# Kernel optimization log

Measured on AMD Instinct MI355X. Metric: run time of the kernel, lower is better.

The kernel has to match this reference:

```python
import jax, jax.numpy as jnp
import numpy as np

DIM = 1024
NUM_HEADS = 16
HEAD_DIM = DIM // NUM_HEADS
MLP_HIDDEN = 4 * DIM
SCALE = HEAD_DIM ** -0.5
EPS = 1e-5


def setup_inputs() -> dict:
    key = jax.random.key(0)
    ks = jax.random.split(key, 6)
    s = (2.0 / DIM) ** 0.5
    sd = (2.0 / MLP_HIDDEN) ** 0.5
    return {
        "x": jax.random.normal(ks[0], (2, 2048, DIM), dtype=jnp.float32),
        "attn_qkv_weight": jax.random.normal(ks[1], (3 * DIM, DIM), dtype=jnp.float32) * s,
        "attn_out_weight": jax.random.normal(ks[2], (DIM, DIM), dtype=jnp.float32) * s,
        "norm1_weight": jnp.ones((DIM,), jnp.float32),
        "norm1_bias": jnp.zeros((DIM,), jnp.float32),
        "mlp_gate_weight": jax.random.normal(ks[3], (MLP_HIDDEN, DIM), dtype=jnp.float32) * s,
        "mlp_up_weight": jax.random.normal(ks[4], (MLP_HIDDEN, DIM), dtype=jnp.float32) * s,
        "mlp_down_weight": jax.random.normal(ks[5], (DIM, MLP_HIDDEN), dtype=jnp.float32) * sd,
        "norm2_weight": jnp.ones((DIM,), jnp.float32),
        "norm2_bias": jnp.zeros((DIM,), jnp.float32),
    }


def _layer_norm(x, w, b):
    mean = x.mean(axis=-1, keepdims=True)
    var = jnp.mean(jnp.square(x - mean), axis=-1, keepdims=True)
    return (x - mean) / jnp.sqrt(var + EPS) * w + b


def reference(x, attn_qkv_weight, attn_out_weight, norm1_weight, norm1_bias,
              mlp_gate_weight, mlp_up_weight, mlp_down_weight, norm2_weight, norm2_bias):
    B, S, D = x.shape
    residual1 = x
    xn = _layer_norm(x, norm1_weight, norm1_bias)
    qkv = xn @ attn_qkv_weight.T                      # [B,S,3D]
    qkv = qkv.reshape(B, S, 3, NUM_HEADS, HEAD_DIM).transpose(2, 0, 3, 1, 4)
    q, k, v = qkv[0], qkv[1], qkv[2]                  # [B,H,S,hd]
    scores = jnp.einsum('bhqd,bhkd->bhqk', q, k) * SCALE  # full O(S^2) matrix
    attn = jax.nn.softmax(scores, axis=-1)            # no causal mask (default False)
    out = jnp.einsum('bhqk,bhkd->bhqd', attn, v)      # [B,H,S,hd]
    out = out.transpose(0, 2, 1, 3).reshape(B, S, D)
    x2 = residual1 + out @ attn_out_weight.T
    xn2 = _layer_norm(x2, norm2_weight, norm2_bias)
    gate = xn2 @ mlp_gate_weight.T
    up = xn2 @ mlp_up_weight.T
    hidden = jax.nn.silu(gate) * up
    return x2 + hidden @ mlp_down_weight.T
```

## Files before the change

### kernel.cpp

```cpp
#include <hip/hip_runtime.h>

typedef float f32x4 __attribute__((ext_vector_type(4)));
typedef __bf16 bf16x8 __attribute__((ext_vector_type(8)));
typedef unsigned int u32;

#define DEV __device__ __forceinline__
#define WAITVM(n) asm volatile("s_waitcnt vmcnt(" #n ")" ::: "memory")

DEV void gload_lds16(const void* g, void* l) {
  __builtin_amdgcn_global_load_lds(
      (const __attribute__((address_space(1))) u32*)g,
      (__attribute__((address_space(3))) u32*)l, 16, 0, 0);
}

DEV int xcd_swz(int flat, int nwg) {
  return (flat & 7) * (nwg >> 3) + (flat >> 3);
}

__global__ __launch_bounds__(256) void cvt_bf16(const float* __restrict__ in,
                                                __bf16* __restrict__ o, int n) {
  int i = (blockIdx.x * 256 + threadIdx.x) * 8;
  if (i >= n) return;
  float4 a = *(const float4*)(in + i);
  float4 b = *(const float4*)(in + i + 4);
  union { bf16x8 v; __bf16 e[8]; } u;
  u.e[0] = (__bf16)a.x; u.e[1] = (__bf16)a.y; u.e[2] = (__bf16)a.z; u.e[3] = (__bf16)a.w;
  u.e[4] = (__bf16)b.x; u.e[5] = (__bf16)b.y; u.e[6] = (__bf16)b.z; u.e[7] = (__bf16)b.w;
  *(bf16x8*)(o + i) = u.v;
}

__global__ __launch_bounds__(256) void ln_kernel(const float* __restrict__ x,
                                                 const float* __restrict__ w,
                                                 const float* __restrict__ b,
                                                 __bf16* __restrict__ o) {
  const int row = blockIdx.x, tid = threadIdx.x;
  const float4 v = ((const float4*)(x + (size_t)row * 1024))[tid];
  float s  = v.x + v.y + v.z + v.w;
  float s2 = v.x * v.x + v.y * v.y + v.z * v.z + v.w * v.w;
  for (int off = 32; off; off >>= 1) {
    s  += __shfl_down(s, off);
    s2 += __shfl_down(s2, off);
  }
  __shared__ float rs[4], rs2[4];
  if ((tid & 63) == 0) { rs[tid >> 6] = s; rs2[tid >> 6] = s2; }
  __syncthreads();
  float S = rs[0] + rs[1] + rs[2] + rs[3];
  float S2 = rs2[0] + rs2[1] + rs2[2] + rs2[3];
  float mean = S * (1.0f / 1024.0f);
  float var = S2 * (1.0f / 1024.0f) - mean * mean;
  float inv = rsqrtf(var + 1e-5f);
  const float4 wv = ((const float4*)w)[tid];
  const float4 bv = ((const float4*)b)[tid];
  union { ushort4 u4; __bf16 e[4]; } u;
  u.e[0] = (__bf16)((v.x - mean) * inv * wv.x + bv.x);
  u.e[1] = (__bf16)((v.y - mean) * inv * wv.y + bv.y);
  u.e[2] = (__bf16)((v.z - mean) * inv * wv.z + bv.z);
  u.e[3] = (__bf16)((v.w - mean) * inv * wv.w + bv.w);
  *(ushort4*)(o + (size_t)row * 1024 + tid * 4) = u.u4;
}


template <int EPI, int MI>
__global__ __launch_bounds__(256) void gemm_bt(const __bf16* __restrict__ A,
                                               const __bf16* __restrict__ B,
                                               void* __restrict__ Cout,
                                               const float* __restrict__ Res,
                                               int M, int N, int K) {
  constexpr int BM = MI * 32;
  constexpr int L = MI / 2 + 2;
  __shared__ __align__(16) __bf16 As[2][BM * 32];
  __shared__ __align__(16) __bf16 Bs[2][128 * 32];
  const int tid = threadIdx.x;
  const int lane = tid & 63;
  const int w = tid >> 6;
  const int wr = w >> 1, wc = w & 1;
  const int l15 = lane & 15, g = lane >> 4;

  const int nbx = gridDim.x;
  const int logical = xcd_swz(blockIdx.y * nbx + blockIdx.x, nbx * gridDim.y);
  const int per = 8 * nbx, grp = logical / per, rem = logical % per;
  const int bm = (grp * 8 + (rem & 7)) * BM;
  const int bn = (rem >> 3) * 128;

  f32x4 acc[MI][4] = {};

  auto stage = [&](int buf, int k0) {
#pragma unroll
    for (int p = 0; p < MI / 2; ++p) {
      const int ch = p * 256 + tid;
      const int S = ch >> 6, u = ch & 63;
      gload_lds16(A + (size_t)(bm + S * 16 + (u & 15)) * K + k0 + (u >> 4) * 8,
                  &As[buf][(p * 256 + w * 64) * 8]);
    }
#pragma unroll
    for (int p = 0; p < 2; ++p) {
      const int ch = p * 256 + tid;
      const int S = ch >> 6, u = ch & 63;
      gload_lds16(B + (size_t)(bn + S * 16 + (u & 15)) * K + k0 + (u >> 4) * 8,
                  &Bs[buf][(p * 256 + w * 64) * 8]);
    }
  };

  const int NT = K >> 5;
  stage(0, 0);
  stage(1, 32);

  for (int t = 0; t < NT; ++t) {
    if (t + 1 < NT) {
      if (L == 3) WAITVM(3); else WAITVM(4);
    } else {
      WAITVM(0);
    }
    __syncthreads();
    const int cur = t & 1;
    bf16x8 af[MI], bfr[4];
#pragma unroll
    for (int i = 0; i < MI; ++i)
      af[i] = *(const bf16x8*)(&As[cur][(wr * MI + i) * 512 + lane * 8]);
#pragma unroll
    for (int j = 0; j < 4; ++j)
      bfr[j] = *(const bf16x8*)(&Bs[cur][(wc * 4 + j) * 512 + lane * 8]);
#pragma unroll
    for (int i = 0; i < MI; ++i)
#pragma unroll
      for (int j = 0; j < 4; ++j)
        acc[i][j] = __builtin_amdgcn_mfma_f32_16x16x32_bf16(af[i], bfr[j], acc[i][j], 0, 0, 0);
    __syncthreads();
    if (t + 2 < NT) stage(cur, (t + 2) * 32);
  }

  const int r0 = bm + wr * (MI * 16) + g * 4;
  const int c0 = bn + wc * 64 + l15;
#pragma unroll
  for (int i = 0; i < MI; ++i)
#pragma unroll
    for (int j = 0; j < 4; ++j)
#pragma unroll
      for (int r = 0; r < 4; ++r) {
        const size_t idx = (size_t)(r0 + i * 16 + r) * N + (c0 + j * 16);
        const float v = acc[i][j][r];
        if (EPI == 0) ((__bf16*)Cout)[idx] = (__bf16)v;
        else          ((float*)Cout)[idx] = v + Res[idx];
      }
}

__global__ __launch_bounds__(256, 2) void gemm_mlp(const __bf16* __restrict__ A,
                                                   const __bf16* __restrict__ BG,
                                                   const __bf16* __restrict__ BU,
                                                   __bf16* __restrict__ H,
                                                   int M, int N, int K) {
  __shared__ __align__(16) __bf16 As[2][128 * 32];
  __shared__ __align__(16) __bf16 Bg[2][128 * 32];
  __shared__ __align__(16) __bf16 Bu[2][128 * 32];
  const int tid = threadIdx.x;
  const int lane = tid & 63;
  const int w = tid >> 6;
  const int wr = w >> 1, wc = w & 1;
  const int l15 = lane & 15, g = lane >> 4;

  const int nbx = gridDim.x;
  const int logical = xcd_swz(blockIdx.y * nbx + blockIdx.x, nbx * gridDim.y);
  const int per = 8 * nbx, grp = logical / per, rem = logical % per;
  const int bm = (grp * 8 + (rem & 7)) * 128;
  const int bn = (rem >> 3) * 128;

  f32x4 accg[4][4] = {};
  f32x4 accu[4][4] = {};

  auto stage = [&](int buf, int k0) {
#pragma unroll
    for (int p = 0; p < 2; ++p) {
      const int ch = p * 256 + tid;
      const int S = ch >> 6, u = ch & 63;
      const size_t roff = (size_t)(S * 16 + (u & 15));
      const int coff = (u >> 4) * 8;
      const int dst = (p * 256 + w * 64) * 8;
      gload_lds16(A + ((size_t)bm + roff) * K + k0 + coff, &As[buf][dst]);
      gload_lds16(BG + ((size_t)bn + roff) * K + k0 + coff, &Bg[buf][dst]);
      gload_lds16(BU + ((size_t)bn + roff) * K + k0 + coff, &Bu[buf][dst]);
    }
  };

  const int NT = K >> 5;
  stage(0, 0);
  stage(1, 32);

  for (int t = 0; t < NT; ++t) {
    if (t + 1 < NT) { WAITVM(6); } else { WAITVM(0); }
    __syncthreads();
    const int cur = t & 1;
    bf16x8 af[4], bgf[4], buf_[4];
#pragma unroll
    for (int i = 0; i < 4; ++i)
      af[i] = *(const bf16x8*)(&As[cur][(wr * 4 + i) * 512 + lane * 8]);
#pragma unroll
    for (int j = 0; j < 4; ++j) {
      bgf[j] = *(const bf16x8*)(&Bg[cur][(wc * 4 + j) * 512 + lane * 8]);
      buf_[j] = *(const bf16x8*)(&Bu[cur][(wc * 4 + j) * 512 + lane * 8]);
    }
#pragma unroll
    for (int i = 0; i < 4; ++i)
#pragma unroll
      for (int j = 0; j < 4; ++j) {
        accg[i][j] = __builtin_amdgcn_mfma_f32_16x16x32_bf16(af[i], bgf[j], accg[i][j], 0, 0, 0);
        accu[i][j] = __builtin_amdgcn_mfma_f32_16x16x32_bf16(af[i], buf_[j], accu[i][j], 0, 0, 0);
      }
    __syncthreads();
    if (t + 2 < NT) stage(cur, (t + 2) * 32);
  }

  const int r0 = bm + wr * 64 + g * 4;
  const int c0 = bn + wc * 64 + l15;
#pragma unroll
  for (int i = 0; i < 4; ++i)
#pragma unroll
    for (int j = 0; j < 4; ++j)
#pragma unroll
      for (int r = 0; r < 4; ++r) {
        const float gt = accg[i][j][r];
        const float ut = accu[i][j][r];
        const float h = gt / (1.0f + __expf(-gt)) * ut;
        H[(size_t)(r0 + i * 16 + r) * N + (c0 + j * 16)] = (__bf16)h;
      }
}

__global__ __launch_bounds__(256) void transpose_v(const __bf16* __restrict__ qkv,
                                                   __bf16* __restrict__ vT) {
  const int st = blockIdx.x, bh = blockIdx.y;
  const int b = bh >> 4, h = bh & 15;
  __shared__ __bf16 tile[64][80];
  const int tid = threadIdx.x;
#pragma unroll
  for (int it = 0; it < 2; ++it) {
    const int idx = it * 256 + tid;
    const int r = idx >> 3, c0 = (idx & 7) * 8;
    bf16x8 v = *(const bf16x8*)(qkv + (size_t)(b * 2048 + st * 64 + r) * 3072 + 2048 + h * 64 + c0);
    *(bf16x8*)&tile[r][c0] = v;
  }
  __syncthreads();
#pragma unroll
  for (int it = 0; it < 2; ++it) {
    const int idx = it * 256 + tid;
    const int d = idx >> 3, s0 = (idx & 7) * 8;
    union { bf16x8 v; __bf16 e[8]; } u;
#pragma unroll
    for (int j = 0; j < 8; ++j) u.e[j] = tile[s0 + j][d];
    *(bf16x8*)(vT + (size_t)(bh * 64 + d) * 2048 + st * 64 + s0) = u.v;
  }
}

__global__ __launch_bounds__(256) void attn_kernel(const __bf16* __restrict__ qkv,
                                                   const __bf16* __restrict__ vT,
                                                   __bf16* __restrict__ outp) {
  const int logical = xcd_swz(blockIdx.y * 32 + blockIdx.x, 1024);
  const int qt = logical & 31, bh = logical >> 5;
  const int b = bh >> 4, h = bh & 15;
  const int tid = threadIdx.x, lane = tid & 63, w = tid >> 6;
  const int l15 = lane & 15, g = lane >> 4;
  const float CSC = 0.125f * 1.44269504f;

  __shared__ __align__(16) __bf16 Ks[64 * 64];
  __shared__ __align__(16) __bf16 Vs[64 * 64];
  __shared__ __align__(16) __bf16 Ps[4][16 * 80];

  const int qrow = qt * 64 + w * 16 + l15;
  const size_t qbase = (size_t)(b * 2048 + qrow) * 3072 + h * 64;
  const bf16x8 qf0 = *(const bf16x8*)(qkv + qbase + g * 8);
  const bf16x8 qf1 = *(const bf16x8*)(qkv + qbase + 32 + g * 8);

  f32x4 o_acc[4] = {};
  float l_r[4] = {0.f, 0.f, 0.f, 0.f};

  const size_t kgbase = (size_t)(b * 2048) * 3072 + 1024 + h * 64;
  const size_t vgbase = (size_t)bh * 64 * 2048;

  for (int t = 0; t < 32; ++t) {
    const int kv0 = t * 64;
#pragma unroll
    for (int p = 0; p < 2; ++p) {
      const int ch = p * 256 + w * 64 + lane;
      const int row = ch >> 3, c = ch & 7;
      const int gc = c ^ (row & 7);
      gload_lds16(qkv + kgbase + (size_t)(kv0 + row) * 3072 + gc * 8, Ks + (p * 256 + w * 64) * 8);
      gload_lds16(vT + vgbase + (size_t)row * 2048 + kv0 + gc * 8, Vs + (p * 256 + w * 64) * 8);
    }
    asm volatile("s_waitcnt vmcnt(0)" ::: "memory");
    __syncthreads();

    f32x4 sf[4];
    __builtin_amdgcn_s_setprio(1);
#pragma unroll
    for (int ni = 0; ni < 4; ++ni) {
      const int krow = ni * 16 + l15;
      const __bf16* kb = Ks + krow * 64;
      const bf16x8 kf0 = *(const bf16x8*)(kb + ((g ^ (krow & 7)) * 8));
      const bf16x8 kf1 = *(const bf16x8*)(kb + (((4 + g) ^ (krow & 7)) * 8));
      f32x4 z = {0.f, 0.f, 0.f, 0.f};
      z = __builtin_amdgcn_mfma_f32_16x16x32_bf16(qf0, kf0, z, 0, 0, 0);
      z = __builtin_amdgcn_mfma_f32_16x16x32_bf16(qf1, kf1, z, 0, 0, 0);
      sf[ni] = z;
    }
    __builtin_amdgcn_s_setprio(0);

#pragma unroll
    for (int ni = 0; ni < 4; ++ni)
#pragma unroll
      for (int r = 0; r < 4; ++r) {
        const float pv = exp2f(sf[ni][r] * CSC);
        sf[ni][r] = pv;
        l_r[r] += pv;
      }

    __bf16* pw = Ps[w];
#pragma unroll
    for (int ni = 0; ni < 4; ++ni)
#pragma unroll
      for (int r = 0; r < 4; ++r) {
        const int row = g * 4 + r;
        const int pc = (ni * 2 + (l15 >> 3)) ^ (row & 7);
        pw[row * 80 + pc * 8 + (l15 & 7)] = (__bf16)sf[ni][r];
      }
    asm volatile("" ::: "memory");
    const bf16x8 pa0 = *(const bf16x8*)(pw + l15 * 80 + ((g ^ (l15 & 7)) * 8));
    const bf16x8 pa1 = *(const bf16x8*)(pw + l15 * 80 + (((4 + g) ^ (l15 & 7)) * 8));

    __builtin_amdgcn_s_setprio(1);
#pragma unroll
    for (int ni = 0; ni < 4; ++ni) {
      const int vrow = ni * 16 + l15;
      const __bf16* vb = Vs + vrow * 64;
      const bf16x8 vf0 = *(const bf16x8*)(vb + ((g ^ (vrow & 7)) * 8));
      const bf16x8 vf1 = *(const bf16x8*)(vb + (((4 + g) ^ (vrow & 7)) * 8));
      o_acc[ni] = __builtin_amdgcn_mfma_f32_16x16x32_bf16(pa0, vf0, o_acc[ni], 0, 0, 0);
      o_acc[ni] = __builtin_amdgcn_mfma_f32_16x16x32_bf16(pa1, vf1, o_acc[ni], 0, 0, 0);
    }
    __builtin_amdgcn_s_setprio(0);
    __syncthreads();
  }

#pragma unroll
  for (int mk = 1; mk < 16; mk <<= 1)
#pragma unroll
    for (int r = 0; r < 4; ++r) l_r[r] += __shfl_xor(l_r[r], mk);
#pragma unroll
  for (int r = 0; r < 4; ++r) {
    const int orow = qt * 64 + w * 16 + g * 4 + r;
    const float invl = 1.0f / l_r[r];
#pragma unroll
    for (int ni = 0; ni < 4; ++ni)
      outp[(size_t)(b * 2048 + orow) * 1024 + h * 64 + ni * 16 + l15] =
          (__bf16)(o_acc[ni][r] * invl);
  }
}

extern "C" void kernel_launch(void* const* d_in, const int* in_sizes, int n_in,
                              void* d_out, int out_size, void* d_ws, size_t ws_size,
                              hipStream_t stream) {
  const float* x     = (const float*)d_in[0];
  const float* Wqkv  = (const float*)d_in[1];
  const float* Wout  = (const float*)d_in[2];
  const float* n1w   = (const float*)d_in[3];
  const float* n1b   = (const float*)d_in[4];
  const float* Wgate = (const float*)d_in[5];
  const float* Wup   = (const float*)d_in[6];
  const float* Wdown = (const float*)d_in[7];
  const float* n2w   = (const float*)d_in[8];
  const float* n2b   = (const float*)d_in[9];
  float* out = (float*)d_out;
  char* ws = (char*)d_ws;
  const size_t MB = 1u << 20;

  __bf16* XN  = (__bf16*)(ws + 0);
  __bf16* QKV = (__bf16*)(ws + 8 * MB);
  __bf16* VT  = (__bf16*)(ws + 32 * MB);
  __bf16* ATT = (__bf16*)(ws + 40 * MB);
  float*  X2  = (float*)(ws + 48 * MB);
  __bf16* H   = QKV;
  __bf16* WQ  = (__bf16*)(ws + 64 * MB);
  __bf16* WO  = (__bf16*)(ws + 70 * MB);
  __bf16* WG  = (__bf16*)(ws + 72 * MB);
  __bf16* WU  = (__bf16*)(ws + 80 * MB);
  __bf16* WD  = (__bf16*)(ws + 88 * MB);

  cvt_bf16<<<3145728 / 2048, 256, 0, stream>>>(Wqkv, WQ, 3145728);
  cvt_bf16<<<1048576 / 2048, 256, 0, stream>>>(Wout, WO, 1048576);
  cvt_bf16<<<4194304 / 2048, 256, 0, stream>>>(Wgate, WG, 4194304);
  cvt_bf16<<<4194304 / 2048, 256, 0, stream>>>(Wup, WU, 4194304);
  cvt_bf16<<<4194304 / 2048, 256, 0, stream>>>(Wdown, WD, 4194304);

  ln_kernel<<<4096, 256, 0, stream>>>(x, n1w, n1b, XN);
  gemm_bt<0, 4><<<dim3(24, 32), 256, 0, stream>>>(XN, WQ, QKV, nullptr, 4096, 3072, 1024);
  transpose_v<<<dim3(32, 32), 256, 0, stream>>>(QKV, VT);
  attn_kernel<<<dim3(32, 32), 256, 0, stream>>>(QKV, VT, ATT);
  gemm_bt<1, 2><<<dim3(8, 64), 256, 0, stream>>>(ATT, WO, X2, x, 4096, 1024, 1024);
  ln_kernel<<<4096, 256, 0, stream>>>(X2, n2w, n2b, XN);
  gemm_mlp<<<dim3(32, 32), 256, 0, stream>>>(XN, WG, WU, H, 4096, 4096, 1024);
  gemm_bt<1, 2><<<dim3(8, 64), 256, 0, stream>>>(H, WD, out, X2, 4096, 1024, 4096);

  (void)in_sizes; (void)n_in; (void)out_size; (void)ws_size;
}
```

Measured before the change: 383.0 us.

## Restructure GEMM double-buffer loop to single barrier with one-ahead prefetch

Both GEMM kernels (gemm_bt and gemm_mlp) move from a two-tile-ahead prefetch, with partial vmcnt waits and two barriers per K step, to a one-ahead prefetch. The next tile's global-to-LDS loads are issued into the other buffer before the current tile's MFMAs, then the loop waits for vmcnt(0) and hits a single barrier. This removes one __syncthreads per iteration and simplifies the wait counting. In exchange the prefetch depth is shorter, so less memory latency is hidden behind the small per-tile MFMA work. The attention kernel only swaps its inline asm for the new macro.

```diff
diff --git a/kernel.cpp b/kernel.cpp
--- a/kernel.cpp
+++ b/kernel.cpp
@@ -5,7 +5,7 @@
 typedef unsigned int u32;
 
 #define DEV __device__ __forceinline__
-#define WAITVM(n) asm volatile("s_waitcnt vmcnt(" #n ")" ::: "memory")
+#define WAITVM0 asm volatile("s_waitcnt vmcnt(0)" ::: "memory")
 
 DEV void gload_lds16(const void* g, void* l) {
   __builtin_amdgcn_global_load_lds(
@@ -67,7 +67,6 @@
                                                const float* __restrict__ Res,
                                                int M, int N, int K) {
   constexpr int BM = MI * 32;
-  constexpr int L = MI / 2 + 2;
   __shared__ __align__(16) __bf16 As[2][BM * 32];
   __shared__ __align__(16) __bf16 Bs[2][128 * 32];
   const int tid = threadIdx.x;
@@ -101,18 +100,14 @@
     }
   };
 
-  const int NT = K >> 5;
   stage(0, 0);
-  stage(1, 32);
-
-  for (int t = 0; t < NT; ++t) {
-    if (t + 1 < NT) {
-      if (L == 3) WAITVM(3); else WAITVM(4);
-    } else {
-      WAITVM(0);
-    }
-    __syncthreads();
-    const int cur = t & 1;
+  WAITVM0;
+  __syncthreads();
+
+  int cur = 0;
+  for (int k0 = 0;;) {
+    const int nk = k0 + 32;
+    if (nk < K) stage(cur ^ 1, nk);
     bf16x8 af[MI], bfr[4];
 #pragma unroll
     for (int i = 0; i < MI; ++i)
@@ -125,8 +120,11 @@
 #pragma unroll
       for (int j = 0; j < 4; ++j)
         acc[i][j] = __builtin_amdgcn_mfma_f32_16x16x32_bf16(af[i], bfr[j], acc[i][j], 0, 0, 0);
+    if (nk >= K) break;
+    WAITVM0;
     __syncthreads();
-    if (t + 2 < NT) stage(cur, (t + 2) * 32);
+    cur ^= 1;
+    k0 = nk;
   }
 
   const int r0 = bm + wr * (MI * 16) + g * 4;
@@ -181,14 +179,14 @@
     }
   };
 
-  const int NT = K >> 5;
   stage(0, 0);
-  stage(1, 32);
-
-  for (int t = 0; t < NT; ++t) {
-    if (t + 1 < NT) { WAITVM(6); } else { WAITVM(0); }
-    __syncthreads();
-    const int cur = t & 1;
+  WAITVM0;
+  __syncthreads();
+
+  int cur = 0;
+  for (int k0 = 0;;) {
+    const int nk = k0 + 32;
+    if (nk < K) stage(cur ^ 1, nk);
     bf16x8 af[4], bgf[4], buf_[4];
 #pragma unroll
     for (int i = 0; i < 4; ++i)
@@ -205,8 +203,11 @@
         accg[i][j] = __builtin_amdgcn_mfma_f32_16x16x32_bf16(af[i], bgf[j], accg[i][j], 0, 0, 0);
         accu[i][j] = __builtin_amdgcn_mfma_f32_16x16x32_bf16(af[i], buf_[j], accu[i][j], 0, 0, 0);
       }
+    if (nk >= K) break;
+    WAITVM0;
     __syncthreads();
-    if (t + 2 < NT) stage(cur, (t + 2) * 32);
+    cur ^= 1;
+    k0 = nk;
   }
 
   const int r0 = bm + wr * 64 + g * 4;
@@ -284,7 +285,7 @@
       gload_lds16(qkv + kgbase + (size_t)(kv0 + row) * 3072 + gc * 8, Ks + (p * 256 + w * 64) * 8);
       gload_lds16(vT + vgbase + (size_t)row * 2048 + kv0 + gc * 8, Vs + (p * 256 + w * 64) * 8);
     }
-    asm volatile("s_waitcnt vmcnt(0)" ::: "memory");
+    WAITVM0;
     __syncthreads();
 
     f32x4 sf[4];
```

Result: slower. 422.7 us (+10.4%).

## Triple-buffer GEMM LDS stages with single barrier and row-major swizzled tiles

Applied to the files above, without the earlier changes.

The two GEMM kernels move from double to triple LDS buffering. The next-next tile is now issued right after a single barrier at the top of each iteration, which removes the second __syncthreads per K step. Global loads are changed to fetch row-contiguous 64-byte chunks with an XOR-style column rotation, and fragment reads use a matching swizzle to avoid LDS bank conflicts. The grouped block-to-tile mapping is replaced by a plain row-major mapping, and the extra LDS per block may reduce occupancy.

```diff
diff --git a/kernel.cpp b/kernel.cpp
--- a/kernel.cpp
+++ b/kernel.cpp
@@ -67,20 +67,18 @@
                                                const float* __restrict__ Res,
                                                int M, int N, int K) {
   constexpr int BM = MI * 32;
-  constexpr int L = MI / 2 + 2;
-  __shared__ __align__(16) __bf16 As[2][BM * 32];
-  __shared__ __align__(16) __bf16 Bs[2][128 * 32];
+  __shared__ __align__(16) __bf16 As[3][BM * 32];
+  __shared__ __align__(16) __bf16 Bs[3][128 * 32];
   const int tid = threadIdx.x;
   const int lane = tid & 63;
   const int w = tid >> 6;
   const int wr = w >> 1, wc = w & 1;
   const int l15 = lane & 15, g = lane >> 4;
+  const int c8 = ((g + (l15 >> 1)) & 3) * 8;
 
   const int nbx = gridDim.x;
   const int logical = xcd_swz(blockIdx.y * nbx + blockIdx.x, nbx * gridDim.y);
-  const int per = 8 * nbx, grp = logical / per, rem = logical % per;
-  const int bm = (grp * 8 + (rem & 7)) * BM;
-  const int bn = (rem >> 3) * 128;
+  const int bm = (logical / nbx) * BM, bn = (logical % nbx) * 128;
 
   f32x4 acc[MI][4] = {};
 
@@ -88,15 +86,17 @@
 #pragma unroll
     for (int p = 0; p < MI / 2; ++p) {
       const int ch = p * 256 + tid;
-      const int S = ch >> 6, u = ch & 63;
-      gload_lds16(A + (size_t)(bm + S * 16 + (u & 15)) * K + k0 + (u >> 4) * 8,
+      const int row = ch >> 2;
+      const int gc = ((ch & 3) - ((ch >> 3) & 3)) & 3;
+      gload_lds16(A + (size_t)(bm + row) * K + k0 + gc * 8,
                   &As[buf][(p * 256 + w * 64) * 8]);
     }
 #pragma unroll
     for (int p = 0; p < 2; ++p) {
       const int ch = p * 256 + tid;
-      const int S = ch >> 6, u = ch & 63;
-      gload_lds16(B + (size_t)(bn + S * 16 + (u & 15)) * K + k0 + (u >> 4) * 8,
+      const int row = ch >> 2;
+      const int gc = ((ch & 3) - ((ch >> 3) & 3)) & 3;
+      gload_lds16(B + (size_t)(bn + row) * K + k0 + gc * 8,
                   &Bs[buf][(p * 256 + w * 64) * 8]);
     }
   };
@@ -105,28 +105,31 @@
   stage(0, 0);
   stage(1, 32);
 
+  int cur = 0;
   for (int t = 0; t < NT; ++t) {
     if (t + 1 < NT) {
-      if (L == 3) WAITVM(3); else WAITVM(4);
+      if constexpr (MI == 4) { WAITVM(4); } else { WAITVM(3); }
     } else {
       WAITVM(0);
     }
-    __syncthreads();
-    const int cur = t & 1;
+    __builtin_amdgcn_s_barrier();
+    if (t + 2 < NT) {
+      int sb = cur + 2; if (sb >= 3) sb -= 3;
+      stage(sb, (t + 2) * 32);
+    }
     bf16x8 af[MI], bfr[4];
 #pragma unroll
     for (int i = 0; i < MI; ++i)
-      af[i] = *(const bf16x8*)(&As[cur][(wr * MI + i) * 512 + lane * 8]);
+      af[i] = *(const bf16x8*)(&As[cur][(wr * (MI * 16) + i * 16 + l15) * 32 + c8]);
 #pragma unroll
     for (int j = 0; j < 4; ++j)
-      bfr[j] = *(const bf16x8*)(&Bs[cur][(wc * 4 + j) * 512 + lane * 8]);
+      bfr[j] = *(const bf16x8*)(&Bs[cur][(wc * 64 + j * 16 + l15) * 32 + c8]);
 #pragma unroll
     for (int i = 0; i < MI; ++i)
 #pragma unroll
       for (int j = 0; j < 4; ++j)
         acc[i][j] = __builtin_amdgcn_mfma_f32_16x16x32_bf16(af[i], bfr[j], acc[i][j], 0, 0, 0);
-    __syncthreads();
-    if (t + 2 < NT) stage(cur, (t + 2) * 32);
+    cur = (cur == 2) ? 0 : cur + 1;
   }
 
   const int r0 = bm + wr * (MI * 16) + g * 4;
@@ -149,20 +152,19 @@
                                                    const __bf16* __restrict__ BU,
                                                    __bf16* __restrict__ H,
                                                    int M, int N, int K) {
-  __shared__ __align__(16) __bf16 As[2][128 * 32];
-  __shared__ __align__(16) __bf16 Bg[2][128 * 32];
-  __shared__ __align__(16) __bf16 Bu[2][128 * 32];
+  __shared__ __align__(16) __bf16 As[3][128 * 32];
+  __shared__ __align__(16) __bf16 Bg[3][128 * 32];
+  __shared__ __align__(16) __bf16 Bu[3][128 * 32];
   const int tid = threadIdx.x;
   const int lane = tid & 63;
   const int w = tid >> 6;
   const int wr = w >> 1, wc = w & 1;
   const int l15 = lane & 15, g = lane >> 4;
+  const int c8 = ((g + (l15 >> 1)) & 3) * 8;
 
   const int nbx = gridDim.x;
   const int logical = xcd_swz(blockIdx.y * nbx + blockIdx.x, nbx * gridDim.y);
-  const int per = 8 * nbx, grp = logical / per, rem = logical % per;
-  const int bm = (grp * 8 + (rem & 7)) * 128;
-  const int bn = (rem >> 3) * 128;
+  const int bm = (logical / nbx) * 128, bn = (logical % nbx) * 128;
 
   f32x4 accg[4][4] = {};
   f32x4 accu[4][4] = {};
@@ -171,13 +173,13 @@
 #pragma unroll
     for (int p = 0; p < 2; ++p) {
       const int ch = p * 256 + tid;
-      const int S = ch >> 6, u = ch & 63;
-      const size_t roff = (size_t)(S * 16 + (u & 15));
-      const int coff = (u >> 4) * 8;
+      const int row = ch >> 2;
+      const int gc = ((ch & 3) - ((ch >> 3) & 3)) & 3;
+      const int coff = gc * 8;
       const int dst = (p * 256 + w * 64) * 8;
-      gload_lds16(A + ((size_t)bm + roff) * K + k0 + coff, &As[buf][dst]);
-      gload_lds16(BG + ((size_t)bn + roff) * K + k0 + coff, &Bg[buf][dst]);
-      gload_lds16(BU + ((size_t)bn + roff) * K + k0 + coff, &Bu[buf][dst]);
+      gload_lds16(A + (size_t)(bm + row) * K + k0 + coff, &As[buf][dst]);
+      gload_lds16(BG + (size_t)(bn + row) * K + k0 + coff, &Bg[buf][dst]);
+      gload_lds16(BU + (size_t)(bn + row) * K + k0 + coff, &Bu[buf][dst]);
     }
   };
 
@@ -185,18 +187,22 @@
   stage(0, 0);
   stage(1, 32);
 
+  int cur = 0;
   for (int t = 0; t < NT; ++t) {
     if (t + 1 < NT) { WAITVM(6); } else { WAITVM(0); }
-    __syncthreads();
-    const int cur = t & 1;
+    __builtin_amdgcn_s_barrier();
+    if (t + 2 < NT) {
+      int sb = cur + 2; if (sb >= 3) sb -= 3;
+      stage(sb, (t + 2) * 32);
+    }
     bf16x8 af[4], bgf[4], buf_[4];
 #pragma unroll
     for (int i = 0; i < 4; ++i)
-      af[i] = *(const bf16x8*)(&As[cur][(wr * 4 + i) * 512 + lane * 8]);
+      af[i] = *(const bf16x8*)(&As[cur][(wr * 64 + i * 16 + l15) * 32 + c8]);
 #pragma unroll
     for (int j = 0; j < 4; ++j) {
-      bgf[j] = *(const bf16x8*)(&Bg[cur][(wc * 4 + j) * 512 + lane * 8]);
-      buf_[j] = *(const bf16x8*)(&Bu[cur][(wc * 4 + j) * 512 + lane * 8]);
+      bgf[j] = *(const bf16x8*)(&Bg[cur][(wc * 64 + j * 16 + l15) * 32 + c8]);
+      buf_[j] = *(const bf16x8*)(&Bu[cur][(wc * 64 + j * 16 + l15) * 32 + c8]);
     }
 #pragma unroll
     for (int i = 0; i < 4; ++i)
@@ -205,8 +211,7 @@
         accg[i][j] = __builtin_amdgcn_mfma_f32_16x16x32_bf16(af[i], bgf[j], accg[i][j], 0, 0, 0);
         accu[i][j] = __builtin_amdgcn_mfma_f32_16x16x32_bf16(af[i], buf_[j], accu[i][j], 0, 0, 0);
       }
-    __syncthreads();
-    if (t + 2 < NT) stage(cur, (t + 2) * 32);
+    cur = (cur == 2) ? 0 : cur + 1;
   }
 
   const int r0 = bm + wr * 64 + g * 4;
@@ -284,7 +289,7 @@
       gload_lds16(qkv + kgbase + (size_t)(kv0 + row) * 3072 + gc * 8, Ks + (p * 256 + w * 64) * 8);
       gload_lds16(vT + vgbase + (size_t)row * 2048 + kv0 + gc * 8, Vs + (p * 256 + w * 64) * 8);
     }
-    asm volatile("s_waitcnt vmcnt(0)" ::: "memory");
+    WAITVM(0);
     __syncthreads();
 
     f32x4 sf[4];
```

Result: faster. 312.0 us (-18.5%).

## Give each wave private LDS tiles to drop block barriers in GEMMs

Applied to the files above, without the earlier changes.

The bf16 GEMM and fused gate/up MLP kernels now have each wave stage its own A and B sub-tiles into a private LDS region with a rotated-column swizzle. This lets the two __syncthreads per k-step be replaced by per-wave vmcnt/lgkmcnt waits. The cost is redundant global loads, since A rows are shared by the two column waves and B rows by the two row waves, plus more LDS per block; gemm_mlp also drops its occupancy hint of 2. The grouped block-rasterisation is replaced with simple row-major tile order, and an unused EPI==2 silu-multiply epilogue is added.

```diff
diff --git a/kernel.cpp b/kernel.cpp
--- a/kernel.cpp
+++ b/kernel.cpp
@@ -6,6 +6,7 @@
 
 #define DEV __device__ __forceinline__
 #define WAITVM(n) asm volatile("s_waitcnt vmcnt(" #n ")" ::: "memory")
+#define WAITLGKM0 asm volatile("s_waitcnt lgkmcnt(0)" ::: "memory")
 
 DEV void gload_lds16(const void* g, void* l) {
   __builtin_amdgcn_global_load_lds(
@@ -67,37 +68,36 @@
                                                const float* __restrict__ Res,
                                                int M, int N, int K) {
   constexpr int BM = MI * 32;
-  constexpr int L = MI / 2 + 2;
-  __shared__ __align__(16) __bf16 As[2][BM * 32];
-  __shared__ __align__(16) __bf16 Bs[2][128 * 32];
+  __shared__ __align__(16) __bf16 As[4][2][MI * 16 * 32];
+  __shared__ __align__(16) __bf16 Bs[4][2][64 * 32];
   const int tid = threadIdx.x;
   const int lane = tid & 63;
   const int w = tid >> 6;
   const int wr = w >> 1, wc = w & 1;
   const int l15 = lane & 15, g = lane >> 4;
+  const int c8 = ((g + (l15 >> 1)) & 3) * 8;
 
   const int nbx = gridDim.x;
   const int logical = xcd_swz(blockIdx.y * nbx + blockIdx.x, nbx * gridDim.y);
-  const int per = 8 * nbx, grp = logical / per, rem = logical % per;
-  const int bm = (grp * 8 + (rem & 7)) * BM;
-  const int bn = (rem >> 3) * 128;
+  const int bm = (logical / nbx) * BM, bn = (logical % nbx) * 128;
+
+  const __bf16* Abase = A + (size_t)(bm + wr * (MI * 16)) * K;
+  const __bf16* Bbase = B + (size_t)(bn + wc * 64) * K;
 
   f32x4 acc[MI][4] = {};
 
   auto stage = [&](int buf, int k0) {
 #pragma unroll
-    for (int p = 0; p < MI / 2; ++p) {
-      const int ch = p * 256 + tid;
-      const int S = ch >> 6, u = ch & 63;
-      gload_lds16(A + (size_t)(bm + S * 16 + (u & 15)) * K + k0 + (u >> 4) * 8,
-                  &As[buf][(p * 256 + w * 64) * 8]);
-    }
-#pragma unroll
-    for (int p = 0; p < 2; ++p) {
-      const int ch = p * 256 + tid;
-      const int S = ch >> 6, u = ch & 63;
-      gload_lds16(B + (size_t)(bn + S * 16 + (u & 15)) * K + k0 + (u >> 4) * 8,
-                  &Bs[buf][(p * 256 + w * 64) * 8]);
+    for (int it = 0; it < MI; ++it) {
+      const int s = it * 64 + lane;
+      const int gc = ((s & 3) - ((s >> 3) & 3)) & 3;
+      gload_lds16(Abase + (size_t)(s >> 2) * K + k0 + gc * 8, &As[w][buf][it * 512]);
+    }
+#pragma unroll
+    for (int it = 0; it < 4; ++it) {
+      const int s = it * 64 + lane;
+      const int gc = ((s & 3) - ((s >> 3) & 3)) & 3;
+      gload_lds16(Bbase + (size_t)(s >> 2) * K + k0 + gc * 8, &Bs[w][buf][it * 512]);
     }
   };
 
@@ -106,26 +106,25 @@
   stage(1, 32);
 
   for (int t = 0; t < NT; ++t) {
-    if (t + 1 < NT) {
-      if (L == 3) WAITVM(3); else WAITVM(4);
+    if (t < NT - 1) {
+      if constexpr (MI == 4) { WAITVM(8); } else { WAITVM(6); }
     } else {
       WAITVM(0);
     }
-    __syncthreads();
     const int cur = t & 1;
     bf16x8 af[MI], bfr[4];
 #pragma unroll
     for (int i = 0; i < MI; ++i)
-      af[i] = *(const bf16x8*)(&As[cur][(wr * MI + i) * 512 + lane * 8]);
+      af[i] = *(const bf16x8*)(&As[w][cur][(i * 16 + l15) * 32 + c8]);
 #pragma unroll
     for (int j = 0; j < 4; ++j)
-      bfr[j] = *(const bf16x8*)(&Bs[cur][(wc * 4 + j) * 512 + lane * 8]);
+      bfr[j] = *(const bf16x8*)(&Bs[w][cur][(j * 16 + l15) * 32 + c8]);
 #pragma unroll
     for (int i = 0; i < MI; ++i)
 #pragma unroll
       for (int j = 0; j < 4; ++j)
         acc[i][j] = __builtin_amdgcn_mfma_f32_16x16x32_bf16(af[i], bfr[j], acc[i][j], 0, 0, 0);
-    __syncthreads();
+    WAITLGKM0;
     if (t + 2 < NT) stage(cur, (t + 2) * 32);
   }
 
@@ -139,45 +138,53 @@
       for (int r = 0; r < 4; ++r) {
         const size_t idx = (size_t)(r0 + i * 16 + r) * N + (c0 + j * 16);
         const float v = acc[i][j][r];
-        if (EPI == 0) ((__bf16*)Cout)[idx] = (__bf16)v;
-        else          ((float*)Cout)[idx] = v + Res[idx];
+        if (EPI == 0) {
+          ((__bf16*)Cout)[idx] = (__bf16)v;
+        } else if (EPI == 1) {
+          ((float*)Cout)[idx] = v + Res[idx];
+        } else {
+          __bf16* C = (__bf16*)Cout;
+          const float gt = (float)C[idx];
+          C[idx] = (__bf16)(gt / (1.0f + __expf(-gt)) * v);
+        }
       }
 }
 
-__global__ __launch_bounds__(256, 2) void gemm_mlp(const __bf16* __restrict__ A,
-                                                   const __bf16* __restrict__ BG,
-                                                   const __bf16* __restrict__ BU,
-                                                   __bf16* __restrict__ H,
-                                                   int M, int N, int K) {
-  __shared__ __align__(16) __bf16 As[2][128 * 32];
-  __shared__ __align__(16) __bf16 Bg[2][128 * 32];
-  __shared__ __align__(16) __bf16 Bu[2][128 * 32];
+__global__ __launch_bounds__(256) void gemm_mlp(const __bf16* __restrict__ A,
+                                                const __bf16* __restrict__ BG,
+                                                const __bf16* __restrict__ BU,
+                                                __bf16* __restrict__ H,
+                                                int M, int N, int K) {
+  __shared__ __align__(16) __bf16 As[4][2][64 * 32];
+  __shared__ __align__(16) __bf16 Bg[4][2][64 * 32];
+  __shared__ __align__(16) __bf16 Bu[4][2][64 * 32];
   const int tid = threadIdx.x;
   const int lane = tid & 63;
   const int w = tid >> 6;
   const int wr = w >> 1, wc = w & 1;
   const int l15 = lane & 15, g = lane >> 4;
+  const int c8 = ((g + (l15 >> 1)) & 3) * 8;
 
   const int nbx = gridDim.x;
   const int logical = xcd_swz(blockIdx.y * nbx + blockIdx.x, nbx * gridDim.y);
-  const int per = 8 * nbx, grp = logical / per, rem = logical % per;
-  const int bm = (grp * 8 + (rem & 7)) * 128;
-  const int bn = (rem >> 3) * 128;
+  const int bm = (logical / nbx) * 128, bn = (logical % nbx) * 128;
+
+  const __bf16* Abase = A + (size_t)(bm + wr * 64) * K;
+  const __bf16* Gbase = BG + (size_t)(bn + wc * 64) * K;
+  const __bf16* Ubase = BU + (size_t)(bn + wc * 64) * K;
 
   f32x4 accg[4][4] = {};
   f32x4 accu[4][4] = {};
 
   auto stage = [&](int buf, int k0) {
 #pragma unroll
-    for (int p = 0; p < 2; ++p) {
-      const int ch = p * 256 + tid;
-      const int S = ch >> 6, u = ch & 63;
-      const size_t roff = (size_t)(S * 16 + (u & 15));
-      const int coff = (u >> 4) * 8;
-      const int dst = (p * 256 + w * 64) * 8;
-      gload_lds16(A + ((size_t)bm + roff) * K + k0 + coff, &As[buf][dst]);
-      gload_lds16(BG + ((size_t)bn + roff) * K + k0 + coff, &Bg[buf][dst]);
-      gload_lds16(BU + ((size_t)bn + roff) * K + k0 + coff, &Bu[buf][dst]);
+    for (int it = 0; it < 4; ++it) {
+      const int s = it * 64 + lane;
+      const int gc = ((s & 3) - ((s >> 3) & 3)) & 3;
+      const size_t ro = (size_t)(s >> 2) * K + k0 + gc * 8;
+      gload_lds16(Abase + ro, &As[w][buf][it * 512]);
+      gload_lds16(Gbase + ro, &Bg[w][buf][it * 512]);
+      gload_lds16(Ubase + ro, &Bu[w][buf][it * 512]);
     }
   };
 
@@ -186,17 +193,16 @@
   stage(1, 32);
 
   for (int t = 0; t < NT; ++t) {
-    if (t + 1 < NT) { WAITVM(6); } else { WAITVM(0); }
-    __syncthreads();
+    if (t < NT - 1) { WAITVM(12); } else { WAITVM(0); }
     const int cur = t & 1;
     bf16x8 af[4], bgf[4], buf_[4];
 #pragma unroll
     for (int i = 0; i < 4; ++i)
-      af[i] = *(const bf16x8*)(&As[cur][(wr * 4 + i) * 512 + lane * 8]);
+      af[i] = *(const bf16x8*)(&As[w][cur][(i * 16 + l15) * 32 + c8]);
 #pragma unroll
     for (int j = 0; j < 4; ++j) {
-      bgf[j] = *(const bf16x8*)(&Bg[cur][(wc * 4 + j) * 512 + lane * 8]);
-      buf_[j] = *(const bf16x8*)(&Bu[cur][(wc * 4 + j) * 512 + lane * 8]);
+      bgf[j] = *(const bf16x8*)(&Bg[w][cur][(j * 16 + l15) * 32 + c8]);
+      buf_[j] = *(const bf16x8*)(&Bu[w][cur][(j * 16 + l15) * 32 + c8]);
     }
 #pragma unroll
     for (int i = 0; i < 4; ++i)
@@ -205,7 +211,7 @@
         accg[i][j] = __builtin_amdgcn_mfma_f32_16x16x32_bf16(af[i], bgf[j], accg[i][j], 0, 0, 0);
         accu[i][j] = __builtin_amdgcn_mfma_f32_16x16x32_bf16(af[i], buf_[j], accu[i][j], 0, 0, 0);
       }
-    __syncthreads();
+    WAITLGKM0;
     if (t + 2 < NT) stage(cur, (t + 2) * 32);
   }
 
@@ -219,8 +225,8 @@
       for (int r = 0; r < 4; ++r) {
         const float gt = accg[i][j][r];
         const float ut = accu[i][j][r];
-        const float h = gt / (1.0f + __expf(-gt)) * ut;
-        H[(size_t)(r0 + i * 16 + r) * N + (c0 + j * 16)] = (__bf16)h;
+        H[(size_t)(r0 + i * 16 + r) * N + (c0 + j * 16)] =
+            (__bf16)(gt / (1.0f + __expf(-gt)) * ut);
       }
 }
 
@@ -284,7 +290,7 @@
       gload_lds16(qkv + kgbase + (size_t)(kv0 + row) * 3072 + gc * 8, Ks + (p * 256 + w * 64) * 8);
       gload_lds16(vT + vgbase + (size_t)row * 2048 + kv0 + gc * 8, Vs + (p * 256 + w * 64) * 8);
     }
-    asm volatile("s_waitcnt vmcnt(0)" ::: "memory");
+    WAITVM(0);
     __syncthreads();
 
     f32x4 sf[4];
```

Result: faster. 372.1 us (-2.8%).
